# Optimization experiments

Measured on AMD Instinct MI355X. Metric: run time of the kernel, lower is better.

## Reference

```python
import jax, jax.numpy as jnp
import numpy as np
from jax import lax

B, L, E = 16, 100, 128
NQ, NC, DL = 1000, 100, 100
NODE, PATH, MAXC = 5000, 5000, 128


def setup_inputs() -> dict:
    key = jax.random.key(0)
    ks = jax.random.split(key, 40)
    rn = lambda k, *s: jax.random.normal(k, s, jnp.float32) * 0.02
    inp = {}
    inp['code'] = jax.random.randint(ks[0], (B, L, NQ * 2 + MAXC * 3), 0, NODE, jnp.int32)
    inp['q'] = jax.random.randint(ks[1], (B, L), 0, NQ, jnp.int32)
    inp['c'] = jax.random.randint(ks[2], (B, L), 0, NC, jnp.int32)
    inp['sd'] = jax.random.randint(ks[3], (B, L), 0, DL, jnp.int32)
    inp['qd'] = jax.random.randint(ks[4], (B, L), 0, DL, jnp.int32)
    inp['a'] = jax.random.randint(ks[5], (B, L), 0, NQ * 2, jnp.int32)
    inp['qshft'] = jax.random.randint(ks[6], (B, L), 0, NQ, jnp.int32)
    inp['cshft'] = jax.random.randint(ks[7], (B, L), 0, NC, jnp.int32)
    inp['sdshft'] = jax.random.randint(ks[8], (B, L), 0, DL, jnp.int32)
    inp['qdshft'] = jax.random.randint(ks[9], (B, L), 0, DL, jnp.int32)
    # embedding tables (padding rows zeroed, matching torch padding_idx)
    inp['embed_nodes'] = rn(ks[10], NODE + 2, E)
    inp['embed_paths'] = rn(ks[11], PATH + 2, E)
    inp['q_tab'] = rn(ks[12], NQ + 1, E).at[NQ].set(0.0)
    inp['c_tab'] = rn(ks[13], NC + 1, E).at[NC].set(0.0)
    inp['sd_tab'] = rn(ks[14], DL + 100, E).at[0].set(0.0)
    inp['qd_tab'] = rn(ks[15], DL + 100, E).at[0].set(0.0)
    inp['a_tab'] = rn(ks[16], NQ * 2 + 2, E).at[2].set(0.0)
    inp['knowledge'] = rn(ks[17], 1, E)
    # linear weights stored [in, out] so y = x @ W + b
    inp['Wpt'] = rn(ks[18], 3 * E, 3 * E); inp['bpt'] = rn(ks[19], 3 * E)
    inp['Wat'] = rn(ks[20], 3 * E, 1);     inp['bat'] = rn(ks[21], 1)
    inp['Wqa'] = rn(ks[22], 4 * E, E);     inp['bqa'] = rn(ks[23], E)
    inp['W1'] = rn(ks[24], 4 * E, E);      inp['b1'] = rn(ks[25], E)
    inp['W2'] = rn(ks[26], E, E);          inp['b2'] = rn(ks[27], E)
    inp['W3'] = rn(ks[28], E, E);          inp['b3'] = rn(ks[29], E)
    inp['W4'] = rn(ks[30], 2 * E, E);      inp['b4'] = rn(ks[31], E)
    inp['W5'] = rn(ks[32], 2 * E, E);      inp['b5'] = rn(ks[33], E)
    inp['W6'] = rn(ks[34], 4 * E, E);      inp['b6'] = rn(ks[35], E)
    inp['Wf'] = rn(ks[36], E, 10);         inp['bf'] = rn(ks[37], 10)
    return inp


def reference(code, q, c, sd, qd, a, qshft, cshft, sdshft, qdshft,
              embed_nodes, embed_paths, q_tab, c_tab, sd_tab, qd_tab, a_tab,
              knowledge, Wpt, bpt, Wat, bat, Wqa, bqa, W1, b1, W2, b2, W3, b3,
              W4, b4, W5, b5, W6, b6, Wf, bf):
    Bq, Lq = q.shape
    # ---- code2vec attention over AST paths ----
    c2v = code[:, :, NQ * 2:].reshape(Bq, Lq, MAXC, 3)
    full = jnp.concatenate([embed_nodes[c2v[..., 0]],
                            embed_nodes[c2v[..., 2]],
                            embed_paths[c2v[..., 1]]], axis=-1)  # [B,L,MAXC,3E]
    tr = jnp.tanh(full @ Wpt + bpt)
    ctx = tr @ Wat + bat                      # [B,L,MAXC,1]
    attn = jax.nn.softmax(ctx, axis=1)        # softmax over seq dim (dim=1), as in source
    code_vec = jnp.sum(full * attn, axis=2)   # [B,L,3E]
    # ---- embeddings + input projections ----
    a_e = a_tab[a]
    acode = jnp.concatenate([a_e, code_vec], axis=-1) @ Wqa + bqa   # [B,L,E]
    inp = jnp.concatenate([q_tab[q], c_tab[c], sd_tab[sd], qd_tab[qd]], axis=-1) @ W1 + b1
    sd_e = sd_tab[sd]
    qd_e = qd_tab[qd]
    # ---- sequential SDF/PKA/KSU recurrence ----
    k0 = jnp.tile(knowledge, (Bq, 1))  # [B,E]

    def step(k, ts):
        inp_t, a_t, sd_t, qd_t = ts
        qq = inp_t - k
        sdf = jax.nn.sigmoid(qq @ W2 + b2) * jnp.tanh(qq @ W3 + b3)
        x = jnp.concatenate([sdf, a_t], axis=-1)
        pka = jax.nn.sigmoid(x @ W4 + b4) * jnp.tanh(x @ W5 + b5)
        ins = jnp.concatenate([k, a_t, sd_t, qd_t], axis=-1)
        g = jax.nn.sigmoid(ins @ W6 + b6)
        k_new = g * k + (1.0 - g) * pka
        return k_new, k_new @ Wf + bf

    xs = (inp.transpose(1, 0, 2), acode.transpose(1, 0, 2),
          sd_e.transpose(1, 0, 2), qd_e.transpose(1, 0, 2))
    _, logits = lax.scan(step, k0, xs)        # [L,B,10]
    return jax.nn.sigmoid(logits.transpose(1, 0, 2))  # [B,L,10]
```

## Files before the change

kernel.cpp:

```cpp
#include <hip/hip_runtime.h>
#include <hip/hip_bf16.h>

#define B_   16
#define L_   100
#define E_   128
#define NQ_  1000
#define MAXC_ 128
#define CODE_STRIDE (NQ_*2 + MAXC_*3)
#define CODE_OFF    (NQ_*2)

typedef short bf16x8 __attribute__((ext_vector_type(8)));
typedef float f32x4  __attribute__((ext_vector_type(4)));

__device__ __forceinline__ unsigned short f2b(float f) {
    unsigned u = __float_as_uint(f);
    unsigned r = (u + 0x7fffu + ((u >> 16) & 1u)) >> 16;
    return (unsigned short)r;
}
__device__ __forceinline__ unsigned cvt2(float lo, float hi) {
    unsigned r;
    asm("v_cvt_pk_bf16_f32 %0, %1, %2" : "=v"(r) : "v"(lo), "v"(hi));
    return r;
}
__device__ __forceinline__ float fsig(float x) {
    return __builtin_amdgcn_rcpf(1.0f + __builtin_amdgcn_exp2f(-1.44269504f * x));
}
__device__ __forceinline__ float ftanh(float x) {
    return 1.0f - 2.0f * __builtin_amdgcn_rcpf(1.0f + __builtin_amdgcn_exp2f(2.88539008f * x));
}
__device__ __forceinline__ void ldsbar() {
    asm volatile("s_waitcnt lgkmcnt(0)" ::: "memory");
    __builtin_amdgcn_s_barrier();
}
__device__ __forceinline__ void gll16(const void* g, void* l) {
    __builtin_amdgcn_global_load_lds(
        (const __attribute__((address_space(1))) unsigned int*)g,
        (__attribute__((address_space(3))) unsigned int*)l, 16, 0, 0);
}

__global__ void k_prep(const float* __restrict__ Wpt, const float* __restrict__ en,
                       const float* __restrict__ ep,
                       const float* __restrict__ W2, const float* __restrict__ W3,
                       const float* __restrict__ W4, const float* __restrict__ W5,
                       const float* __restrict__ W6, const float* __restrict__ Wf,
                       const float* __restrict__ Wqa, const float* __restrict__ W1,
                       unsigned short* __restrict__ wptT, unsigned short* __restrict__ enb,
                       unsigned short* __restrict__ epb, unsigned short* __restrict__ bt1,
                       unsigned short* __restrict__ bt2, unsigned short* __restrict__ btf,
                       unsigned short* __restrict__ bW1, unsigned short* __restrict__ bW2,
                       unsigned short* __restrict__ bW6)
{
    int i = blockIdx.x * 256 + threadIdx.x;
    switch (blockIdx.y) {
    case 0: if (i < 384*384) {
                int e = i & 7, G = i >> 3;
                int l15g = G & 15, rest = G >> 4;
                int l4g = rest & 3, rest2 = rest >> 2;
                int ksg = rest2 % 12, tile = rest2 / 12;
                int n = tile*16 + l15g, k = ksg*32 + l4g*8 + e;
                wptT[i] = f2b(Wpt[k*384 + n]);
            } break;
    case 1: if (i < 5002*128) enb[i] = f2b(en[i]); break;
    case 2: if (i < 5002*128) epb[i] = f2b(ep[i]); break;
    case 3: if (i < 384*128) {
                int n = i >> 7, k = i & 127;
                float v = (n < 128) ? W2[k*128 + n] : (n < 256) ? W3[k*128 + (n-128)]
                                                                : W6[k*128 + (n-256)];
                bt1[i] = f2b(v);
            } break;
    case 4: if (i < 256*128) {
                int n = i >> 7, k = i & 127;
                float v = (n < 128) ? W4[k*128 + n] : W5[k*128 + (n-128)];
                bt2[i] = f2b(v);
            } break;
    case 5: if (i < 16*128) {
                int n = i >> 7, k = i & 127;
                btf[i] = f2b(n < 10 ? Wf[k*10 + n] : 0.0f);
            } break;
    case 6: if (i < 256*512) {
                int n = i >> 9, k = i & 511;
                float v = (n < 128) ? Wqa[k*128 + n] : W1[k*128 + (n-128)];
                bW1[i] = f2b(v);
            } break;
    case 7: if (i < 512*128) {
                int n = i >> 7, k = i & 127;
                float v = (n < 128) ? W2[k*128 + n]
                        : (n < 256) ? W3[k*128 + (n-128)]
                        : (n < 384) ? W4[(128 + k)*128 + (n-256)]
                                    : W5[(128 + k)*128 + (n-384)];
                bW2[i] = f2b(v);
            } break;
    case 8: if (i < 128*384) {
                int n = i / 384, k = i % 384;
                bW6[i] = f2b(W6[(128 + k)*128 + n]);
            } break;
    }
}

__global__ __launch_bounds__(256, 3) void k_ctx(const int* __restrict__ code,
    const unsigned short* __restrict__ enb, const unsigned short* __restrict__ epb,
    const unsigned short* __restrict__ wptT, const float* __restrict__ bpt,
    const float* __restrict__ wat, const float* __restrict__ bat,
    float* __restrict__ ctx)
{
    __shared__ __align__(16) unsigned short Bs[3][6144];
    __shared__ float bw[768];
    const int tid = threadIdx.x, wv = tid >> 6, lane = tid & 63;
    const int l15 = lane & 15, l4 = lane >> 4;
    const int rowg0 = blockIdx.x * 128;

    for (int idx = tid; idx < 768; idx += 256)
        bw[idx] = (idx < 384) ? bpt[idx] : wat[idx - 384];

    bf16x8 af[2][12];
    #pragma unroll
    for (int h = 0; h < 2; ++h) {
        int rowg = rowg0 + h * 64 + wv * 16 + l15;
        int m = rowg & 127, bl = rowg >> 7;
        const int* cp = code + (size_t)bl * CODE_STRIDE + CODE_OFF + m * 3;
        int i0 = cp[0], i1 = cp[1], i2 = cp[2];
        #pragma unroll
        for (int ks = 0; ks < 12; ++ks) {
            int seg = ks >> 2;
            int idx = (seg == 0) ? i0 : (seg == 1 ? i2 : i1);
            const unsigned short* tab = (seg == 2) ? epb : enb;
            af[h][ks] = *(const bf16x8*)(tab + (size_t)idx * 128 + (ks & 3) * 32 + l4 * 8);
        }
    }

    #pragma unroll
    for (int c = 0; c < 2; ++c) {
        const unsigned short* src = wptT + c * 6144;
        #pragma unroll
        for (int i = 0; i < 3; ++i) {
            int jj = wv * 3 + i;
            gll16(src + jj * 512 + lane * 8, &Bs[c][jj * 512]);
        }
    }

    float cr[2][4] = {{0.f,0.f,0.f,0.f},{0.f,0.f,0.f,0.f}};
    const float bat0 = bat[0];

    int buf = 0;
    for (int nc = 0; nc < 24; ++nc) {
        if (nc < 23) asm volatile("s_waitcnt vmcnt(3) lgkmcnt(0)" ::: "memory");
        else         asm volatile("s_waitcnt vmcnt(0) lgkmcnt(0)" ::: "memory");
        __builtin_amdgcn_s_barrier();
        if (nc < 22) {
            int nb = buf + 2; if (nb >= 3) nb -= 3;
            const unsigned short* src = wptT + (size_t)(nc + 2) * 6144;
            #pragma unroll
            for (int i = 0; i < 3; ++i) {
                int jj = wv * 3 + i;
                gll16(src + jj * 512 + lane * 8, &Bs[nb][jj * 512]);
            }
        }
        const char* bb0 = (const char*)&Bs[buf][0] + l15 * 16;
        f32x4 acc0 = {0.f,0.f,0.f,0.f}, acc1 = {0.f,0.f,0.f,0.f};
        #pragma unroll
        for (int ks = 0; ks < 12; ++ks) {
            bf16x8 b0 = *(const bf16x8*)(bb0 + (ks * 4 + l4) * 256);
            acc0 = __builtin_amdgcn_mfma_f32_16x16x32_bf16(af[0][ks], b0, acc0, 0, 0, 0);
            acc1 = __builtin_amdgcn_mfma_f32_16x16x32_bf16(af[1][ks], b0, acc1, 0, 0, 0);
        }
        int ng = nc * 16 + l15;
        float bv = bw[ng], wa = bw[384 + ng];
        #pragma unroll
        for (int r = 0; r < 4; ++r) {
            cr[0][r] += ftanh(acc0[r] + bv) * wa;
            cr[1][r] += ftanh(acc1[r] + bv) * wa;
        }
        ++buf; if (buf >= 3) buf = 0;
    }

    #pragma unroll
    for (int h = 0; h < 2; ++h)
        #pragma unroll
        for (int r = 0; r < 4; ++r) {
            float v = cr[h][r];
            v += __shfl_xor(v, 1); v += __shfl_xor(v, 2);
            v += __shfl_xor(v, 4); v += __shfl_xor(v, 8);
            cr[h][r] = v;
        }
    if (l15 == 0) {
        #pragma unroll
        for (int h = 0; h < 2; ++h) {
            int rbase = rowg0 + h * 64 + wv * 16 + l4 * 4;
            #pragma unroll
            for (int r = 0; r < 4; ++r) ctx[rbase + r] = cr[h][r] + bat0;
        }
    }
}

__global__ __launch_bounds__(128) void k_smred(const float* __restrict__ ctx,
    float* __restrict__ mxv, float* __restrict__ inv)
{
    int b = blockIdx.x, m = threadIdx.x;
    const float* p = ctx + (size_t)b * L_ * MAXC_ + m;
    float mx = -1e30f;
    for (int l = 0; l < L_; ++l) mx = fmaxf(mx, p[l * MAXC_]);
    float s = 0.f;
    for (int l = 0; l < L_; ++l)
        s += __builtin_amdgcn_exp2f((p[l * MAXC_] - mx) * 1.44269504f);
    mxv[b * MAXC_ + m] = mx;
    inv[b * MAXC_ + m] = __builtin_amdgcn_rcpf(s);
}

__global__ __launch_bounds__(192) void k_codevec(const int* __restrict__ code,
    const float* __restrict__ ctx, const float* __restrict__ mxv,
    const float* __restrict__ inv, const unsigned short* __restrict__ enb,
    const unsigned short* __restrict__ epb, float* __restrict__ cv)
{
    __shared__ float sm[128];
    int bl = blockIdx.x;
    int t = threadIdx.x;
    int b = bl / 100;
    if (t < 128) {
        float v = ctx[(size_t)bl * MAXC_ + t];
        sm[t] = __builtin_amdgcn_exp2f((v - mxv[b * MAXC_ + t]) * 1.44269504f)
                * inv[b * MAXC_ + t];
    }
    ldsbar();
    int seg = t >> 6, tc = t & 63;
    const int* cp = code + (size_t)bl * CODE_STRIDE + CODE_OFF;
    const unsigned short* tab = (seg == 2) ? epb : enb;
    const int sidx = (seg == 0) ? 0 : (seg == 1) ? 2 : 1;
    float ax = 0.f, ay = 0.f;
    #pragma unroll 8
    for (int m = 0; m < MAXC_; ++m) {
        float w = sm[m];
        int idx = cp[m * 3 + sidx];
        unsigned u = *((const unsigned*)(tab + (size_t)idx * 128) + tc);
        ax += w * __uint_as_float(u << 16);
        ay += w * __uint_as_float(u & 0xffff0000u);
    }
    float2 o; o.x = ax; o.y = ay;
    *(float2*)(cv + (size_t)bl * 384 + seg * 128 + tc * 2) = o;
}

__global__ __launch_bounds__(256) void k_fuse(
    const int* __restrict__ a, const int* __restrict__ q, const int* __restrict__ c,
    const int* __restrict__ sd, const int* __restrict__ qd,
    const float* __restrict__ a_tab, const float* __restrict__ q_tab,
    const float* __restrict__ c_tab, const float* __restrict__ sd_tab,
    const float* __restrict__ qd_tab, const float* __restrict__ cv,
    const unsigned short* __restrict__ bW1, const unsigned short* __restrict__ bW2,
    const unsigned short* __restrict__ bW6,
    const float* __restrict__ bqa, const float* __restrict__ b1,
    const float* __restrict__ b2, const float* __restrict__ b3,
    const float* __restrict__ b4, const float* __restrict__ b5,
    const float* __restrict__ b6,
    float4* __restrict__ preQ, float* __restrict__ pre6)
{
    __shared__ __align__(16) unsigned short X[16 * 1024];
    __shared__ __align__(16) unsigned short Y[16 * 256];
    const int tid = threadIdx.x, wv = tid >> 6, lane = tid & 63;
    const int l15 = lane & 15, l4 = lane >> 4;
    const int row0 = blockIdx.x * 16;

    #pragma unroll
    for (int it = 0; it < 16; ++it) {
        int idx = tid + it * 256;
        int r = idx >> 8, col = (idx & 255) * 4;
        int row = row0 + r;
        const float* src;
        if (col < 128)       src = a_tab + (size_t)a[row] * 128 + col;
        else if (col < 512)  src = cv + (size_t)row * 384 + (col - 128);
        else if (col < 640)  src = q_tab + (size_t)q[row] * 128 + (col - 512);
        else if (col < 768)  src = c_tab + (size_t)c[row] * 128 + (col - 640);
        else if (col < 896)  src = sd_tab + (size_t)sd[row] * 128 + (col - 768);
        else                 src = qd_tab + (size_t)qd[row] * 128 + (col - 896);
        float4 v = *(const float4*)src;
        unsigned u0 = cvt2(v.x, v.y), u1 = cvt2(v.z, v.w);
        int byte = r * 2048 + ((((col >> 3)) ^ (r & 7)) << 4) + ((col & 4) << 1);
        *(unsigned*)((char*)X + byte) = u0;
        *(unsigned*)((char*)X + byte + 4) = u1;
    }
    ldsbar();

    {
        bf16x8 ak[16];
        int kbase = (wv < 2) ? 0 : 512;
        #pragma unroll
        for (int ks = 0; ks < 16; ++ks) {
            int col = kbase + ks * 32 + l4 * 8;
            ak[ks] = *(const bf16x8*)((const char*)X + l15 * 2048 + (((col >> 3) ^ (l15 & 7)) << 4));
        }
        int nbase = wv * 64;
        f32x4 acc[4] = {{0,0,0,0},{0,0,0,0},{0,0,0,0},{0,0,0,0}};
        #pragma unroll
        for (int i = 0; i < 4; ++i) {
            const unsigned short* bp = bW1 + (size_t)(nbase + i * 16 + l15) * 512 + l4 * 8;
            #pragma unroll
            for (int ks = 0; ks < 16; ++ks) {
                bf16x8 bfr = *(const bf16x8*)(bp + ks * 32);
                acc[i] = __builtin_amdgcn_mfma_f32_16x16x32_bf16(ak[ks], bfr, acc[i], 0, 0, 0);
            }
        }
        #pragma unroll
        for (int i = 0; i < 4; ++i) {
            int cc = nbase + i * 16 + l15;
            float bias = (cc < 128) ? bqa[cc] : b1[cc - 128];
            #pragma unroll
            for (int rr = 0; rr < 4; ++rr) {
                int row = l4 * 4 + rr;
                int byte = row * 512 + (((cc >> 3) ^ (row & 7)) << 4) + (cc & 7) * 2;
                *(unsigned short*)((char*)Y + byte) = f2b(acc[i][rr] + bias);
            }
        }
    }
    ldsbar();

    bf16x8 zi[4], za[4], zs[4], zq[4];
    #pragma unroll
    for (int ks = 0; ks < 4; ++ks) {
        int ci = 128 + ks * 32 + l4 * 8;
        zi[ks] = *(const bf16x8*)((const char*)Y + l15 * 512 + (((ci >> 3) ^ (l15 & 7)) << 4));
        int ca = ks * 32 + l4 * 8;
        za[ks] = *(const bf16x8*)((const char*)Y + l15 * 512 + (((ca >> 3) ^ (l15 & 7)) << 4));
        int cs = 768 + ks * 32 + l4 * 8;
        zs[ks] = *(const bf16x8*)((const char*)X + l15 * 2048 + (((cs >> 3) ^ (l15 & 7)) << 4));
        int cq = 896 + ks * 32 + l4 * 8;
        zq[ks] = *(const bf16x8*)((const char*)X + l15 * 2048 + (((cq >> 3) ^ (l15 & 7)) << 4));
    }
    f32x4 A2[2] = {{0,0,0,0},{0,0,0,0}}, A3[2] = {{0,0,0,0},{0,0,0,0}};
    f32x4 A4[2] = {{0,0,0,0},{0,0,0,0}}, A5[2] = {{0,0,0,0},{0,0,0,0}};
    f32x4 A6[2] = {{0,0,0,0},{0,0,0,0}};
    #pragma unroll
    for (int tt = 0; tt < 2; ++tt) {
        int n = wv * 32 + tt * 16 + l15;
        const unsigned short* p2 = bW2 + (size_t)(      n) * 128 + l4 * 8;
        const unsigned short* p3 = bW2 + (size_t)(128 + n) * 128 + l4 * 8;
        const unsigned short* p4 = bW2 + (size_t)(256 + n) * 128 + l4 * 8;
        const unsigned short* p5 = bW2 + (size_t)(384 + n) * 128 + l4 * 8;
        const unsigned short* p6 = bW6 + (size_t)n * 384 + l4 * 8;
        #pragma unroll
        for (int ks = 0; ks < 4; ++ks) {
            A2[tt] = __builtin_amdgcn_mfma_f32_16x16x32_bf16(zi[ks], *(const bf16x8*)(p2 + ks*32), A2[tt], 0, 0, 0);
            A3[tt] = __builtin_amdgcn_mfma_f32_16x16x32_bf16(zi[ks], *(const bf16x8*)(p3 + ks*32), A3[tt], 0, 0, 0);
            A4[tt] = __builtin_amdgcn_mfma_f32_16x16x32_bf16(za[ks], *(const bf16x8*)(p4 + ks*32), A4[tt], 0, 0, 0);
            A5[tt] = __builtin_amdgcn_mfma_f32_16x16x32_bf16(za[ks], *(const bf16x8*)(p5 + ks*32), A5[tt], 0, 0, 0);
            A6[tt] = __builtin_amdgcn_mfma_f32_16x16x32_bf16(za[ks], *(const bf16x8*)(p6 + ks*32), A6[tt], 0, 0, 0);
        }
        #pragma unroll
        for (int ks = 0; ks < 4; ++ks)
            A6[tt] = __builtin_amdgcn_mfma_f32_16x16x32_bf16(zs[ks], *(const bf16x8*)(p6 + 256 + ks*32), A6[tt], 0, 0, 0);
        #pragma unroll
        for (int ks = 0; ks < 4; ++ks)
            A6[tt] = __builtin_amdgcn_mfma_f32_16x16x32_bf16(zq[ks], *(const bf16x8*)(p6 + 512 + ks*32), A6[tt], 0, 0, 0);
    }
    #pragma unroll
    for (int tt = 0; tt < 2; ++tt) {
        int n = wv * 32 + tt * 16 + l15;
        float c2 = b2[n], c3 = b3[n], c4 = b4[n], c5 = b5[n], c6 = b6[n];
        #pragma unroll
        for (int rr = 0; rr < 4; ++rr) {
            size_t row = (size_t)(row0 + l4 * 4 + rr);
            float4 o;
            o.x = A2[tt][rr] + c2; o.y = A3[tt][rr] + c3;
            o.z = A4[tt][rr] + c4; o.w = A5[tt][rr] + c5;
            preQ[row * 128 + n] = o;
            pre6[row * 128 + n] = A6[tt][rr] + c6;
        }
    }
}

__global__ __launch_bounds__(512) void k_recur(
    const unsigned short* __restrict__ bt1, const unsigned short* __restrict__ bt2,
    const float* __restrict__ knowledge, const float4* __restrict__ preQ,
    const float* __restrict__ pre6, unsigned short* __restrict__ khist)
{
    __shared__ __align__(16) unsigned short k_lds[16 * 128];
    __shared__ __align__(16) unsigned short s_lds[16 * 128];
    const int tid = threadIdx.x, wv = tid >> 6, lane = tid & 63;
    const int l15 = lane & 15, l4 = lane >> 4;
    const int j = wv * 16 + l15;

    bf16x8 w2f[4], w3f[4], w6f[4], w4f[4], w5f[4];
    #pragma unroll
    for (int ks = 0; ks < 4; ++ks) {
        w2f[ks] = *(const bf16x8*)(bt1 + (size_t)(      j) * 128 + ks * 32 + l4 * 8);
        w3f[ks] = *(const bf16x8*)(bt1 + (size_t)(128 + j) * 128 + ks * 32 + l4 * 8);
        w6f[ks] = *(const bf16x8*)(bt1 + (size_t)(256 + j) * 128 + ks * 32 + l4 * 8);
        w4f[ks] = *(const bf16x8*)(bt2 + (size_t)(      j) * 128 + ks * 32 + l4 * 8);
        w5f[ks] = *(const bf16x8*)(bt2 + (size_t)(128 + j) * 128 + ks * 32 + l4 * 8);
    }

    float kreg[4], gR[4];
    {
        float k0 = knowledge[j];
        unsigned short kb = f2b(k0);
        #pragma unroll
        for (int r = 0; r < 4; ++r) {
            kreg[r] = k0;
            int b = l4 * 4 + r;
            k_lds[b * 128 + (((j >> 3) ^ b) << 3) + (j & 7)] = kb;
        }
    }
    ldsbar();

    float4 pv[4]; float p6[4];
    #pragma unroll
    for (int r = 0; r < 4; ++r) {
        int b = l4 * 4 + r;
        size_t ix = (size_t)(b * L_) * 128 + j;
        pv[r] = preQ[ix]; p6[r] = pre6[ix];
    }

    for (int t = 0; t < L_; ++t) {
        float4 pvN[4]; float p6N[4];
        #pragma unroll
        for (int r = 0; r < 4; ++r) {
            int b = l4 * 4 + r;
            size_t ix = (size_t)(b * L_ + t + 1) * 128 + j;
            pvN[r] = preQ[ix]; p6N[r] = pre6[ix];
        }

        bf16x8 ak[4];
        {
            const unsigned short* kb = k_lds + l15 * 128;
            #pragma unroll
            for (int ks = 0; ks < 4; ++ks)
                ak[ks] = *(const bf16x8*)(kb + (((ks * 4 + l4) ^ l15) << 3));
        }
        f32x4 a2 = {0,0,0,0}, a3 = {0,0,0,0}, a6 = {0,0,0,0};
        #pragma unroll
        for (int ks = 0; ks < 4; ++ks) {
            a2 = __builtin_amdgcn_mfma_f32_16x16x32_bf16(ak[ks], w2f[ks], a2, 0, 0, 0);
            a3 = __builtin_amdgcn_mfma_f32_16x16x32_bf16(ak[ks], w3f[ks], a3, 0, 0, 0);
            a6 = __builtin_amdgcn_mfma_f32_16x16x32_bf16(ak[ks], w6f[ks], a6, 0, 0, 0);
        }
        #pragma unroll
        for (int r = 0; r < 4; ++r) {
            int b = l4 * 4 + r;
            float sdf = fsig(pv[r].x - a2[r]) * ftanh(pv[r].y - a3[r]);
            gR[r] = fsig(a6[r] + p6[r]);
            s_lds[b * 128 + (((j >> 3) ^ b) << 3) + (j & 7)] = f2b(sdf);
        }
        ldsbar();
        bf16x8 as[4];
        {
            const unsigned short* sb = s_lds + l15 * 128;
            #pragma unroll
            for (int ks = 0; ks < 4; ++ks)
                as[ks] = *(const bf16x8*)(sb + (((ks * 4 + l4) ^ l15) << 3));
        }
        f32x4 a4 = {0,0,0,0}, a5 = {0,0,0,0};
        #pragma unroll
        for (int ks = 0; ks < 4; ++ks) {
            a4 = __builtin_amdgcn_mfma_f32_16x16x32_bf16(as[ks], w4f[ks], a4, 0, 0, 0);
            a5 = __builtin_amdgcn_mfma_f32_16x16x32_bf16(as[ks], w5f[ks], a5, 0, 0, 0);
        }
        #pragma unroll
        for (int r = 0; r < 4; ++r) {
            int b = l4 * 4 + r;
            float pka = fsig(a4[r] + pv[r].z) * ftanh(a5[r] + pv[r].w);
            float kn = gR[r] * kreg[r] + (1.0f - gR[r]) * pka;
            kreg[r] = kn;
            unsigned short kb2 = f2b(kn);
            k_lds[b * 128 + (((j >> 3) ^ b) << 3) + (j & 7)] = kb2;
            khist[(size_t)(b * L_ + t) * 128 + j] = kb2;
        }
        #pragma unroll
        for (int r = 0; r < 4; ++r) { pv[r] = pvN[r]; p6[r] = p6N[r]; }
        ldsbar();
    }
}

__global__ __launch_bounds__(256) void k_logits(const unsigned short* __restrict__ khist,
    const unsigned short* __restrict__ btf, const float* __restrict__ bfv,
    float* __restrict__ out)
{
    int wv = threadIdx.x >> 6, lane = threadIdx.x & 63;
    int l15 = lane & 15, l4 = lane >> 4;
    int R0 = (blockIdx.x * 4 + wv) * 16;
    bf16x8 wbf[4], akr[4];
    #pragma unroll
    for (int ks = 0; ks < 4; ++ks)
        wbf[ks] = *(const bf16x8*)(btf + (size_t)l15 * 128 + ks * 32 + l4 * 8);
    const unsigned short* kb = khist + (size_t)(R0 + l15) * 128;
    #pragma unroll
    for (int ks = 0; ks < 4; ++ks)
        akr[ks] = *(const bf16x8*)(kb + ks * 32 + l4 * 8);
    f32x4 af = {0.f, 0.f, 0.f, 0.f};
    #pragma unroll
    for (int ks = 0; ks < 4; ++ks)
        af = __builtin_amdgcn_mfma_f32_16x16x32_bf16(akr[ks], wbf[ks], af, 0, 0, 0);
    if (l15 < 10) {
        float bb = bfv[l15];
        #pragma unroll
        for (int r = 0; r < 4; ++r)
            out[(size_t)(R0 + l4 * 4 + r) * 10 + l15] = fsig(af[r] + bb);
    }
}

extern "C" void kernel_launch(void* const* d_in, const int* in_sizes, int n_in,
                              void* d_out, int out_size, void* d_ws, size_t ws_size,
                              hipStream_t stream)
{
    const int*   code  = (const int*)d_in[0];
    const int*   q     = (const int*)d_in[1];
    const int*   c     = (const int*)d_in[2];
    const int*   sd    = (const int*)d_in[3];
    const int*   qd    = (const int*)d_in[4];
    const int*   a     = (const int*)d_in[5];
    const float* en    = (const float*)d_in[10];
    const float* ep    = (const float*)d_in[11];
    const float* q_tab = (const float*)d_in[12];
    const float* c_tab = (const float*)d_in[13];
    const float* sd_tab= (const float*)d_in[14];
    const float* qd_tab= (const float*)d_in[15];
    const float* a_tab = (const float*)d_in[16];
    const float* know  = (const float*)d_in[17];
    const float* Wpt   = (const float*)d_in[18];
    const float* bpt   = (const float*)d_in[19];
    const float* Wat   = (const float*)d_in[20];
    const float* bat   = (const float*)d_in[21];
    const float* Wqa   = (const float*)d_in[22];
    const float* bqa   = (const float*)d_in[23];
    const float* W1    = (const float*)d_in[24];
    const float* b1    = (const float*)d_in[25];
    const float* W2    = (const float*)d_in[26];
    const float* b2    = (const float*)d_in[27];
    const float* W3    = (const float*)d_in[28];
    const float* b3    = (const float*)d_in[29];
    const float* W4    = (const float*)d_in[30];
    const float* b4    = (const float*)d_in[31];
    const float* W5    = (const float*)d_in[32];
    const float* b5    = (const float*)d_in[33];
    const float* W6    = (const float*)d_in[34];
    const float* b6    = (const float*)d_in[35];
    const float* Wf    = (const float*)d_in[36];
    const float* bf_   = (const float*)d_in[37];

    char* ws = (char*)d_ws;
    size_t off = 0;
    auto alloc = [&](size_t n) { size_t r = off; off += (n + 255) & ~(size_t)255; return r; };
    unsigned short* wptT = (unsigned short*)(ws + alloc(384 * 384 * 2));
    unsigned short* enb  = (unsigned short*)(ws + alloc(5002 * 128 * 2));
    unsigned short* epb  = (unsigned short*)(ws + alloc(5002 * 128 * 2));
    unsigned short* bt1  = (unsigned short*)(ws + alloc(384 * 128 * 2));
    unsigned short* bt2  = (unsigned short*)(ws + alloc(256 * 128 * 2));
    unsigned short* btf  = (unsigned short*)(ws + alloc(16 * 128 * 2));
    unsigned short* bW1  = (unsigned short*)(ws + alloc(256 * 512 * 2));
    unsigned short* bW2  = (unsigned short*)(ws + alloc(512 * 128 * 2));
    unsigned short* bW6  = (unsigned short*)(ws + alloc(128 * 384 * 2));
    float* ctx   = (float*)(ws + alloc((size_t)B_ * L_ * MAXC_ * 4));
    float* mxv   = (float*)(ws + alloc((size_t)B_ * MAXC_ * 4));
    float* inv   = (float*)(ws + alloc((size_t)B_ * MAXC_ * 4));
    float* cv    = (float*)(ws + alloc((size_t)B_ * L_ * 384 * 4));
    float4* preQ = (float4*)(ws + alloc(((size_t)B_ * L_ * 128 + 128) * 16));
    float* pre6  = (float*)(ws + alloc(((size_t)B_ * L_ * 128 + 128) * 4));
    unsigned short* khist = (unsigned short*)(ws + alloc((size_t)B_ * L_ * 128 * 2));
    float* outf  = (float*)d_out;

    k_prep<<<dim3(2501, 9), 256, 0, stream>>>(Wpt, en, ep, W2, W3, W4, W5, W6, Wf,
                                              Wqa, W1,
                                              wptT, enb, epb, bt1, bt2, btf,
                                              bW1, bW2, bW6);
    k_ctx<<<1600, 256, 0, stream>>>(code, enb, epb, wptT, bpt, Wat, bat, ctx);
    k_smred<<<16, 128, 0, stream>>>(ctx, mxv, inv);
    k_codevec<<<1600, 192, 0, stream>>>(code, ctx, mxv, inv, enb, epb, cv);
    k_fuse<<<100, 256, 0, stream>>>(a, q, c, sd, qd, a_tab, q_tab, c_tab, sd_tab,
                                    qd_tab, cv, bW1, bW2, bW6, bqa, b1,
                                    b2, b3, b4, b5, b6, preQ, pre6);
    k_recur<<<1, 512, 0, stream>>>(bt1, bt2, know, preQ, pre6, khist);
    k_logits<<<25, 256, 0, stream>>>(khist, btf, bf_, outf);
}
```

Measured before the change: 293.1 us.

## Fuse logits projection into recurrence kernel and split MFMA accumulator chains

Moves the final Wf projection and sigmoid into the single-block recurrence kernel. Wave 0 computes the previous step's logits from the k values already in LDS, which removes the khist buffer and the separate k_logits launch. It also splits each MFMA accumulation into two independent chains to shorten dependency latency on the serial critical path. Other changes are precomputing swizzled LDS offsets, using packed bf16 conversion, and rewriting the gate blend. The cost is extra MFMA work for wave 0 on every step of the serial loop, which may add imbalance.

```diff
diff --git a/kernel.cpp b/kernel.cpp
--- a/kernel.cpp
+++ b/kernel.cpp
@@ -367,8 +367,9 @@
 
 __global__ __launch_bounds__(512) void k_recur(
     const unsigned short* __restrict__ bt1, const unsigned short* __restrict__ bt2,
-    const float* __restrict__ knowledge, const float4* __restrict__ preQ,
-    const float* __restrict__ pre6, unsigned short* __restrict__ khist)
+    const unsigned short* __restrict__ btf, const float* __restrict__ knowledge,
+    const float4* __restrict__ preQ, const float* __restrict__ pre6,
+    const float* __restrict__ bfv, float* __restrict__ out)
 {
     __shared__ __align__(16) unsigned short k_lds[16 * 128];
     __shared__ __align__(16) unsigned short s_lds[16 * 128];
@@ -376,7 +377,7 @@
     const int l15 = lane & 15, l4 = lane >> 4;
     const int j = wv * 16 + l15;
 
-    bf16x8 w2f[4], w3f[4], w6f[4], w4f[4], w5f[4];
+    bf16x8 w2f[4], w3f[4], w6f[4], w4f[4], w5f[4], wbf[4];
     #pragma unroll
     for (int ks = 0; ks < 4; ++ks) {
         w2f[ks] = *(const bf16x8*)(bt1 + (size_t)(      j) * 128 + ks * 32 + l4 * 8);
@@ -384,18 +385,22 @@
         w6f[ks] = *(const bf16x8*)(bt1 + (size_t)(256 + j) * 128 + ks * 32 + l4 * 8);
         w4f[ks] = *(const bf16x8*)(bt2 + (size_t)(      j) * 128 + ks * 32 + l4 * 8);
         w5f[ks] = *(const bf16x8*)(bt2 + (size_t)(128 + j) * 128 + ks * 32 + l4 * 8);
-    }
+        wbf[ks] = *(const bf16x8*)(btf + (size_t)l15 * 128 + ks * 32 + l4 * 8);
+    }
+    const float bb = (l15 < 10) ? bfv[l15] : 0.0f;
+
+    int woff[4], roff[4];
+    #pragma unroll
+    for (int r = 0; r < 4; ++r) { int b = l4 * 4 + r; woff[r] = b * 128 + (((j >> 3) ^ b) << 3) + (j & 7); }
+    #pragma unroll
+    for (int ks = 0; ks < 4; ++ks) roff[ks] = l15 * 128 + (((ks * 4 + l4) ^ l15) << 3);
 
     float kreg[4], gR[4];
     {
         float k0 = knowledge[j];
         unsigned short kb = f2b(k0);
         #pragma unroll
-        for (int r = 0; r < 4; ++r) {
-            kreg[r] = k0;
-            int b = l4 * 4 + r;
-            k_lds[b * 128 + (((j >> 3) ^ b) << 3) + (j & 7)] = kb;
-        }
+        for (int r = 0; r < 4; ++r) { kreg[r] = k0; k_lds[woff[r]] = kb; }
     }
     ldsbar();
 
@@ -417,80 +422,106 @@
         }
 
         bf16x8 ak[4];
+        #pragma unroll
+        for (int ks = 0; ks < 4; ++ks)
+            ak[ks] = *(const bf16x8*)(k_lds + roff[ks]);
+
+        if (wv == 0 && t > 0) {
+            f32x4 afa = {0,0,0,0}, afb = {0,0,0,0};
+            afa = __builtin_amdgcn_mfma_f32_16x16x32_bf16(ak[0], wbf[0], afa, 0, 0, 0);
+            afb = __builtin_amdgcn_mfma_f32_16x16x32_bf16(ak[1], wbf[1], afb, 0, 0, 0);
+            afa = __builtin_amdgcn_mfma_f32_16x16x32_bf16(ak[2], wbf[2], afa, 0, 0, 0);
+            afb = __builtin_amdgcn_mfma_f32_16x16x32_bf16(ak[3], wbf[3], afb, 0, 0, 0);
+            if (l15 < 10) {
+                #pragma unroll
+                for (int r = 0; r < 4; ++r)
+                    out[(size_t)((l4 * 4 + r) * L_ + (t - 1)) * 10 + l15] = fsig(afa[r] + afb[r] + bb);
+            }
+        }
+
+        f32x4 a2a = {0,0,0,0}, a2b = {0,0,0,0};
+        f32x4 a3a = {0,0,0,0}, a3b = {0,0,0,0};
+        f32x4 a6a = {0,0,0,0}, a6b = {0,0,0,0};
+        a2a = __builtin_amdgcn_mfma_f32_16x16x32_bf16(ak[0], w2f[0], a2a, 0, 0, 0);
+        a2b = __builtin_amdgcn_mfma_f32_16x16x32_bf16(ak[1], w2f[1], a2b, 0, 0, 0);
+        a3a = __builtin_amdgcn_mfma_f32_16x16x32_bf16(ak[0], w3f[0], a3a, 0, 0, 0);
+        a3b = __builtin_amdgcn_mfma_f32_16x16x32_bf16(ak[1], w3f[1], a3b, 0, 0, 0);
+        a6a = __builtin_amdgcn_mfma_f32_16x16x32_bf16(ak[0], w6f[0], a6a, 0, 0, 0);
+        a6b = __builtin_amdgcn_mfma_f32_16x16x32_bf16(ak[1], w6f[1], a6b, 0, 0, 0);
+        a2a = __builtin_amdgcn_mfma_f32_16x16x32_bf16(ak[2], w2f[2], a2a, 0, 0, 0);
+        a2b = __builtin_amdgcn_mfma_f32_16x16x32_bf16(ak[3], w2f[3], a2b, 0, 0, 0);
+        a3a = __builtin_amdgcn_mfma_f32_16x16x32_bf16(ak[2], w3f[2], a3a, 0, 0, 0);
+        a3b = __builtin_amdgcn_mfma_f32_16x16x32_bf16(ak[3], w3f[3], a3b, 0, 0, 0);
+        a6a = __builtin_amdgcn_mfma_f32_16x16x32_bf16(ak[2], w6f[2], a6a, 0, 0, 0);
+        a6b = __builtin_amdgcn_mfma_f32_16x16x32_bf16(ak[3], w6f[3], a6b, 0, 0, 0);
+
+        float ss[4];
+        #pragma unroll
+        for (int r = 0; r < 4; ++r) {
+            float u2 = a2a[r] + a2b[r], u3 = a3a[r] + a3b[r], u6 = a6a[r] + a6b[r];
+            ss[r] = fsig(pv[r].x - u2) * ftanh(pv[r].y - u3);
+            gR[r] = fsig(u6 + p6[r]);
+        }
         {
-            const unsigned short* kb = k_lds + l15 * 128;
-            #pragma unroll
-            for (int ks = 0; ks < 4; ++ks)
-                ak[ks] = *(const bf16x8*)(kb + (((ks * 4 + l4) ^ l15) << 3));
-        }
-        f32x4 a2 = {0,0,0,0}, a3 = {0,0,0,0}, a6 = {0,0,0,0};
-        #pragma unroll
-        for (int ks = 0; ks < 4; ++ks) {
-            a2 = __builtin_amdgcn_mfma_f32_16x16x32_bf16(ak[ks], w2f[ks], a2, 0, 0, 0);
-            a3 = __builtin_amdgcn_mfma_f32_16x16x32_bf16(ak[ks], w3f[ks], a3, 0, 0, 0);
-            a6 = __builtin_amdgcn_mfma_f32_16x16x32_bf16(ak[ks], w6f[ks], a6, 0, 0, 0);
-        }
+            unsigned su01 = cvt2(ss[0], ss[1]), su23 = cvt2(ss[2], ss[3]);
+            s_lds[woff[0]] = (unsigned short)su01;
+            s_lds[woff[1]] = (unsigned short)(su01 >> 16);
+            s_lds[woff[2]] = (unsigned short)su23;
+            s_lds[woff[3]] = (unsigned short)(su23 >> 16);
+        }
+        ldsbar();
+
+        bf16x8 as[4];
+        #pragma unroll
+        for (int ks = 0; ks < 4; ++ks)
+            as[ks] = *(const bf16x8*)(s_lds + roff[ks]);
+        f32x4 a4a = {0,0,0,0}, a4b = {0,0,0,0};
+        f32x4 a5a = {0,0,0,0}, a5b = {0,0,0,0};
+        a4a = __builtin_amdgcn_mfma_f32_16x16x32_bf16(as[0], w4f[0], a4a, 0, 0, 0);
+        a4b = __builtin_amdgcn_mfma_f32_16x16x32_bf16(as[1], w4f[1], a4b, 0, 0, 0);
+        a5a = __builtin_amdgcn_mfma_f32_16x16x32_bf16(as[0], w5f[0], a5a, 0, 0, 0);
+        a5b = __builtin_amdgcn_mfma_f32_16x16x32_bf16(as[1], w5f[1], a5b, 0, 0, 0);
+        a4a = __builtin_amdgcn_mfma_f32_16x16x32_bf16(as[2], w4f[2], a4a, 0, 0, 0);
+        a4b = __builtin_amdgcn_mfma_f32_16x16x32_bf16(as[3], w4f[3], a4b, 0, 0, 0);
+        a5a = __builtin_amdgcn_mfma_f32_16x16x32_bf16(as[2], w5f[2], a5a, 0, 0, 0);
+        a5b = __builtin_amdgcn_mfma_f32_16x16x32_bf16(as[3], w5f[3], a5b, 0, 0, 0);
+
+        float kn[4];
         #pragma unroll
         for (int r = 0; r < 4; ++r) {
-            int b = l4 * 4 + r;
-            float sdf = fsig(pv[r].x - a2[r]) * ftanh(pv[r].y - a3[r]);
-            gR[r] = fsig(a6[r] + p6[r]);
-            s_lds[b * 128 + (((j >> 3) ^ b) << 3) + (j & 7)] = f2b(sdf);
-        }
-        ldsbar();
-        bf16x8 as[4];
+            float pka = fsig(a4a[r] + a4b[r] + pv[r].z) * ftanh(a5a[r] + a5b[r] + pv[r].w);
+            kn[r] = pka + gR[r] * (kreg[r] - pka);
+            kreg[r] = kn[r];
+        }
         {
-            const unsigned short* sb = s_lds + l15 * 128;
-            #pragma unroll
-            for (int ks = 0; ks < 4; ++ks)
-                as[ks] = *(const bf16x8*)(sb + (((ks * 4 + l4) ^ l15) << 3));
-        }
-        f32x4 a4 = {0,0,0,0}, a5 = {0,0,0,0};
-        #pragma unroll
-        for (int ks = 0; ks < 4; ++ks) {
-            a4 = __builtin_amdgcn_mfma_f32_16x16x32_bf16(as[ks], w4f[ks], a4, 0, 0, 0);
-            a5 = __builtin_amdgcn_mfma_f32_16x16x32_bf16(as[ks], w5f[ks], a5, 0, 0, 0);
-        }
-        #pragma unroll
-        for (int r = 0; r < 4; ++r) {
-            int b = l4 * 4 + r;
-            float pka = fsig(a4[r] + pv[r].z) * ftanh(a5[r] + pv[r].w);
-            float kn = gR[r] * kreg[r] + (1.0f - gR[r]) * pka;
-            kreg[r] = kn;
-            unsigned short kb2 = f2b(kn);
-            k_lds[b * 128 + (((j >> 3) ^ b) << 3) + (j & 7)] = kb2;
-            khist[(size_t)(b * L_ + t) * 128 + j] = kb2;
+            unsigned ku01 = cvt2(kn[0], kn[1]), ku23 = cvt2(kn[2], kn[3]);
+            k_lds[woff[0]] = (unsigned short)ku01;
+            k_lds[woff[1]] = (unsigned short)(ku01 >> 16);
+            k_lds[woff[2]] = (unsigned short)ku23;
+            k_lds[woff[3]] = (unsigned short)(ku23 >> 16);
         }
         #pragma unroll
         for (int r = 0; r < 4; ++r) { pv[r] = pvN[r]; p6[r] = p6N[r]; }
         ldsbar();
     }
-}
-
-__global__ __launch_bounds__(256) void k_logits(const unsigned short* __restrict__ khist,
-    const unsigned short* __restrict__ btf, const float* __restrict__ bfv,
-    float* __restrict__ out)
-{
-    int wv = threadIdx.x >> 6, lane = threadIdx.x & 63;
-    int l15 = lane & 15, l4 = lane >> 4;
-    int R0 = (blockIdx.x * 4 + wv) * 16;
-    bf16x8 wbf[4], akr[4];
-    #pragma unroll
-    for (int ks = 0; ks < 4; ++ks)
-        wbf[ks] = *(const bf16x8*)(btf + (size_t)l15 * 128 + ks * 32 + l4 * 8);
-    const unsigned short* kb = khist + (size_t)(R0 + l15) * 128;
-    #pragma unroll
-    for (int ks = 0; ks < 4; ++ks)
-        akr[ks] = *(const bf16x8*)(kb + ks * 32 + l4 * 8);
-    f32x4 af = {0.f, 0.f, 0.f, 0.f};
-    #pragma unroll
-    for (int ks = 0; ks < 4; ++ks)
-        af = __builtin_amdgcn_mfma_f32_16x16x32_bf16(akr[ks], wbf[ks], af, 0, 0, 0);
-    if (l15 < 10) {
-        float bb = bfv[l15];
-        #pragma unroll
-        for (int r = 0; r < 4; ++r)
-            out[(size_t)(R0 + l4 * 4 + r) * 10 + l15] = fsig(af[r] + bb);
+
+    {
+        bf16x8 ak[4];
+        #pragma unroll
+        for (int ks = 0; ks < 4; ++ks)
+            ak[ks] = *(const bf16x8*)(k_lds + roff[ks]);
+        if (wv == 0) {
+            f32x4 afa = {0,0,0,0}, afb = {0,0,0,0};
+            afa = __builtin_amdgcn_mfma_f32_16x16x32_bf16(ak[0], wbf[0], afa, 0, 0, 0);
+            afb = __builtin_amdgcn_mfma_f32_16x16x32_bf16(ak[1], wbf[1], afb, 0, 0, 0);
+            afa = __builtin_amdgcn_mfma_f32_16x16x32_bf16(ak[2], wbf[2], afa, 0, 0, 0);
+            afb = __builtin_amdgcn_mfma_f32_16x16x32_bf16(ak[3], wbf[3], afb, 0, 0, 0);
+            if (l15 < 10) {
+                #pragma unroll
+                for (int r = 0; r < 4; ++r)
+                    out[(size_t)((l4 * 4 + r) * L_ + (L_ - 1)) * 10 + l15] = fsig(afa[r] + afb[r] + bb);
+            }
+        }
     }
 }
 
@@ -551,7 +582,6 @@
     float* cv    = (float*)(ws + alloc((size_t)B_ * L_ * 384 * 4));
     float4* preQ = (float4*)(ws + alloc(((size_t)B_ * L_ * 128 + 128) * 16));
     float* pre6  = (float*)(ws + alloc(((size_t)B_ * L_ * 128 + 128) * 4));
-    unsigned short* khist = (unsigned short*)(ws + alloc((size_t)B_ * L_ * 128 * 2));
     float* outf  = (float*)d_out;
 
     k_prep<<<dim3(2501, 9), 256, 0, stream>>>(Wpt, en, ep, W2, W3, W4, W5, W6, Wf,
@@ -564,6 +594,5 @@
     k_fuse<<<100, 256, 0, stream>>>(a, q, c, sd, qd, a_tab, q_tab, c_tab, sd_tab,
                                     qd_tab, cv, bW1, bW2, bW6, bqa, b1,
                                     b2, b3, b4, b5, b6, preQ, pre6);
-    k_recur<<<1, 512, 0, stream>>>(bt1, bt2, know, preQ, pre6, khist);
-    k_logits<<<25, 256, 0, stream>>>(khist, btf, bf_, outf);
-}
+    k_recur<<<1, 512, 0, stream>>>(bt1, bt2, btf, know, preQ, pre6, bf_, outf);
+}
```

Measured after the change: 294.9 us. Within noise of the previous version (+0.6%).
